# Kernel tuning notes

Measured on AMD Instinct MI355X. Metric: run time of the kernel, lower is better.

## Reference

```python
import jax, jax.numpy as jnp
import numpy as np

D_MODEL = 2048
NUM_HEADS = 16
D_KV = D_MODEL // NUM_HEADS
THETA = 10000.0


def apply_rope(x, pos):
    # x: [B, H, S, d_kv], pos: [S] int
    d = x.shape[-1]
    inv_freq = 1.0 / (THETA ** (jnp.arange(0, d, 2, dtype=jnp.float32) / d))  # [d/2]
    ang = pos.astype(jnp.float32)[:, None] * inv_freq[None, :]  # [S, d/2]
    cos, sin = jnp.cos(ang), jnp.sin(ang)  # broadcast over B,H
    x1 = x[..., 0::2]
    x2 = x[..., 1::2]
    r1 = x1 * cos - x2 * sin
    r2 = x1 * sin + x2 * cos
    return jnp.stack([r1, r2], axis=-1).reshape(x.shape)


def setup_inputs() -> dict:
    key = jax.random.key(0)
    k = jax.random.split(key, 5)
    B, S = 2, 2048
    x = jax.random.normal(k[0], (B, S, D_MODEL), dtype=jnp.float32)
    scale = 1.0 / np.sqrt(D_MODEL)
    Wq = jax.random.normal(k[1], (D_MODEL, D_MODEL), dtype=jnp.float32) * scale
    Wk = jax.random.normal(k[2], (D_MODEL, D_MODEL), dtype=jnp.float32) * scale
    Wv = jax.random.normal(k[3], (D_MODEL, D_MODEL), dtype=jnp.float32) * scale
    Wo = jax.random.normal(k[4], (D_MODEL, D_MODEL), dtype=jnp.float32) * scale
    token_position = jnp.arange(S, dtype=jnp.int64 if jax.config.jax_enable_x64 else jnp.int32)
    return {"x": x, "Wq": Wq, "Wk": Wk, "Wv": Wv, "Wo": Wo, "token_position": token_position}


def reference(x, Wq, Wk, Wv, Wo, token_position):
    B, S, _ = x.shape
    def heads(y):
        return y.reshape(B, S, NUM_HEADS, D_KV).transpose(0, 2, 1, 3)  # [B,H,S,d]
    Q = heads(jnp.einsum('bsd,df->bsf', x, Wq))
    K = heads(jnp.einsum('bsd,df->bsf', x, Wk))
    V = heads(jnp.einsum('bsd,df->bsf', x, Wv))
    Q = apply_rope(Q, token_position)
    K = apply_rope(K, token_position)
    scale = 1.0 / jnp.sqrt(jnp.asarray(D_KV, dtype=x.dtype))
    scores = jnp.einsum('bhqd,bhkd->bhqk', Q, K) * scale  # [B,H,S,S]
    causal = jnp.tril(jnp.ones((S, S), dtype=bool))
    scores = jnp.where(causal, scores, -jnp.inf)
    attn = jax.nn.softmax(scores, axis=-1)
    out = jnp.einsum('bhqk,bhkd->bhqd', attn, V)  # [B,H,S,d]
    out = out.transpose(0, 2, 1, 3).reshape(B, S, D_MODEL)
    return jnp.einsum('bsd,df->bsf', out, Wo)
```

## Files before the change

### kernel.cpp

```cpp
#include <hip/hip_runtime.h>
#include <hip/hip_bf16.h>

#define S 2048
#define DM 2048
#define NH 16
#define DH 128

typedef __attribute__((ext_vector_type(8))) short short8;
typedef __attribute__((ext_vector_type(4))) float floatx4;
typedef unsigned short u16;
typedef unsigned int u32;

__device__ __forceinline__ u16 f2bf(float f) {
  union { float f; u32 u; } v; v.f = f;
  u32 r = v.u + 0x7fffu + ((v.u >> 16) & 1u);
  return (u16)(r >> 16);
}
__device__ __forceinline__ u32 pack2(float lo, float hi) {
  float2 f; f.x = lo; f.y = hi;
  __hip_bfloat162 h = __float22bfloat162_rn(f);
  union { __hip_bfloat162 h; u32 u; } c; c.h = h;
  return c.u;
}

__device__ __forceinline__ floatx4 mfma16(short8 a, short8 b, floatx4 c) {
  return __builtin_amdgcn_mfma_f32_16x16x32_bf16(a, b, c, 0, 0, 0);
}

__device__ __forceinline__ void async_cp16(const u16* g, u16* l) {
  __builtin_amdgcn_global_load_lds(
      (const __attribute__((address_space(1))) void*)g,
      (__attribute__((address_space(3))) void*)l, 16, 0, 0);
}

__global__ void conv_x_k(const float* __restrict__ x, u16* __restrict__ xb) {
  int gid = blockIdx.x * 256 + threadIdx.x;
  float4 v = ((const float4*)x)[gid];
  uint2 p; p.x = pack2(v.x, v.y); p.y = pack2(v.z, v.w);
  ((uint2*)xb)[gid] = p;
}

__global__ void conv_w_k(const float* __restrict__ W0, const float* __restrict__ W1,
                         const float* __restrict__ W2, const float* __restrict__ W3,
                         u16* __restrict__ out) {
  __shared__ float tile[32][33];
  const float* W = blockIdx.z == 0 ? W0 : blockIdx.z == 1 ? W1 : blockIdx.z == 2 ? W2 : W3;
  u16* O = out + (size_t)blockIdx.z * DM * DM;
  int tx = threadIdx.x & 31, ty = threadIdx.x >> 5;
  int k0 = blockIdx.y * 32, n0 = blockIdx.x * 32;
#pragma unroll
  for (int j = 0; j < 4; j++)
    tile[ty + j * 8][tx] = W[(size_t)(k0 + ty + j * 8) * DM + n0 + tx];
  __syncthreads();
#pragma unroll
  for (int j = 0; j < 4; j++)
    O[(size_t)(n0 + ty + j * 8) * DM + k0 + tx] = f2bf(tile[tx][ty + j * 8]);
}

#define BM 256
#define BN 128
#define BK 64
#define NT (DM / BK)

#define STAGE(p, koff) do {                       \
    async_cp16(pA0 + (koff), &As[p][oA0]);        \
    async_cp16(pA1 + (koff), &As[p][oA1]);        \
    async_cp16(pA2 + (koff), &As[p][oA2]);        \
    async_cp16(pA3 + (koff), &As[p][oA3]);        \
    async_cp16(pB0 + (koff), &Bs[p][oB0]);        \
    async_cp16(pB1 + (koff), &Bs[p][oB1]);        \
  } while (0)

#define PHASE(p, g, F) {                                                  \
    short8 a0k0 = *(const short8*)&As[p][arow64 + (2*(g))*1024 + xk0];    \
    short8 a0k1 = *(const short8*)&As[p][arow64 + (2*(g))*1024 + xk1];    \
    short8 a1k0 = *(const short8*)&As[p][arow64 + (2*(g)+1)*1024 + xk0];  \
    short8 a1k1 = *(const short8*)&As[p][arow64 + (2*(g)+1)*1024 + xk1];  \
    if (F) {                                                              \
      bA = *(const short8*)&Bs[p][brow64 + xk0];                          \
      bB = *(const short8*)&Bs[p][brow64 + xk1];                          \
      bC = *(const short8*)&Bs[p][brow64 + 1024 + xk0];                   \
      bD = *(const short8*)&Bs[p][brow64 + 1024 + xk1];                   \
    }                                                                     \
    __builtin_amdgcn_s_barrier();                                         \
    asm volatile("s_waitcnt lgkmcnt(0)" ::: "memory");                    \
    __builtin_amdgcn_sched_barrier(0);                                    \
    __builtin_amdgcn_s_setprio(1);                                        \
    acc[2*(g)][0]   = mfma16(a0k0, bA, acc[2*(g)][0]);                    \
    acc[2*(g)][1]   = mfma16(a0k0, bC, acc[2*(g)][1]);                    \
    acc[2*(g)+1][0] = mfma16(a1k0, bA, acc[2*(g)+1][0]);                  \
    acc[2*(g)+1][1] = mfma16(a1k0, bC, acc[2*(g)+1][1]);                  \
    acc[2*(g)][0]   = mfma16(a0k1, bB, acc[2*(g)][0]);                    \
    acc[2*(g)][1]   = mfma16(a0k1, bD, acc[2*(g)][1]);                    \
    acc[2*(g)+1][0] = mfma16(a1k1, bB, acc[2*(g)+1][0]);                  \
    acc[2*(g)+1][1] = mfma16(a1k1, bD, acc[2*(g)+1][1]);                  \
    __builtin_amdgcn_s_setprio(0);                                        \
    __builtin_amdgcn_s_barrier();                                         \
  }

#define BOUNDARY(p, koff, pre) {                                          \
    __builtin_amdgcn_sched_barrier(0);                                    \
    if (pre) {                                                            \
      STAGE(p, koff);                                                     \
      __builtin_amdgcn_sched_barrier(0);                                  \
      asm volatile("s_waitcnt vmcnt(6)" ::: "memory");                    \
    } else {                                                              \
      asm volatile("s_waitcnt vmcnt(0)" ::: "memory");                    \
    }                                                                     \
    __builtin_amdgcn_s_barrier();                                         \
    __builtin_amdgcn_sched_barrier(0);                                    \
  }

__global__ __launch_bounds__(512, 2)
void gemm_k(const u16* __restrict__ A, const u16* __restrict__ Wt,
            u16* __restrict__ oQ, u16* __restrict__ oK, u16* __restrict__ oV,
            float* __restrict__ oO, const int* __restrict__ tp, int opmode)
{
  __shared__ u16 As[2][BM * BK];
  __shared__ u16 Bs[2][BN * BK];
  const int t = threadIdx.x;
  const int w = t >> 6, lane = t & 63;
  const int l16 = lane & 15, quad = lane >> 4;
  const int wr = w >> 2, wc = w & 3;
  const int m0 = blockIdx.y * BM, n0 = blockIdx.x * BN;
  const u16* Bt = Wt + (size_t)(opmode == 1 ? 3 : blockIdx.z) * DM * DM;

  int uu, rr, cc;
  uu = t;        rr = uu >> 3; cc = (uu & 7) ^ (rr & 7);
  const u16* pA0 = A + (size_t)(m0 + rr) * DM + cc * 8; const int oA0 = uu * 8;
  uu = t + 512;  rr = uu >> 3; cc = (uu & 7) ^ (rr & 7);
  const u16* pA1 = A + (size_t)(m0 + rr) * DM + cc * 8; const int oA1 = uu * 8;
  uu = t + 1024; rr = uu >> 3; cc = (uu & 7) ^ (rr & 7);
  const u16* pA2 = A + (size_t)(m0 + rr) * DM + cc * 8; const int oA2 = uu * 8;
  uu = t + 1536; rr = uu >> 3; cc = (uu & 7) ^ (rr & 7);
  const u16* pA3 = A + (size_t)(m0 + rr) * DM + cc * 8; const int oA3 = uu * 8;
  uu = t;        rr = uu >> 3; cc = (uu & 7) ^ (rr & 7);
  const u16* pB0 = Bt + (size_t)(n0 + rr) * DM + cc * 8; const int oB0 = uu * 8;
  uu = t + 512;  rr = uu >> 3; cc = (uu & 7) ^ (rr & 7);
  const u16* pB1 = Bt + (size_t)(n0 + rr) * DM + cc * 8; const int oB1 = uu * 8;

  const int arow64 = (wr * 128 + l16) * 64;
  const int brow64 = (wc * 32 + l16) * 64;
  const int xk0 = ((quad) ^ (l16 & 7)) << 3;
  const int xk1 = ((4 + quad) ^ (l16 & 7)) << 3;

  floatx4 acc[8][2] = {};
  short8 bA, bB, bC, bD;

  STAGE(0, 0);
  STAGE(1, BK);
  __builtin_amdgcn_sched_barrier(0);
  asm volatile("s_waitcnt vmcnt(6)" ::: "memory");
  __builtin_amdgcn_s_barrier();
  __builtin_amdgcn_sched_barrier(0);

  for (int it = 0; it < NT / 2; ++it) {
    const int koffE = it * 128 + 128;
    const int koffO = it * 128 + 192;
    const bool pre = (it < NT / 2 - 1);
    PHASE(0, 0, 1) PHASE(0, 1, 0) PHASE(0, 2, 0) PHASE(0, 3, 0)
    BOUNDARY(0, koffE, pre)
    PHASE(1, 0, 1) PHASE(1, 1, 0) PHASE(1, 2, 0) PHASE(1, 3, 0)
    BOUNDARY(1, koffO, pre)
  }

  const int mode = (opmode == 1) ? 3 : ((int)blockIdx.z == 2 ? 2 : 0);
  const int mbase = m0 + wr * 128;
  const int nbase = n0 + wc * 32;
  if (mode == 3) {
#pragma unroll
    for (int mi = 0; mi < 8; mi++) {
      int m = mbase + mi * 16 + quad * 4;
#pragma unroll
      for (int ni = 0; ni < 2; ni++) {
        int n = nbase + ni * 16 + l16;
#pragma unroll
        for (int r = 0; r < 4; r++)
          oO[(size_t)(m + r) * DM + n] = acc[mi][ni][r];
      }
    }
  } else if (mode == 2) {
#pragma unroll
    for (int mi = 0; mi < 8; mi++) {
      int m = mbase + mi * 16 + quad * 4;
      int b = m >> 11, s = m & (S - 1);
#pragma unroll
      for (int ni = 0; ni < 2; ni++) {
        int f = nbase + ni * 16 + l16;
        int h = f >> 7, dh = f & (DH - 1);
        uint2 pk; pk.x = pack2(acc[mi][ni][0], acc[mi][ni][1]);
        pk.y = pack2(acc[mi][ni][2], acc[mi][ni][3]);
        *(uint2*)&oV[((size_t)(b * NH + h) * DH + dh) * S + s] = pk;
      }
    }
  } else {
    u16* Out = ((int)blockIdx.z == 0) ? oQ : oK;
    const float qs = ((int)blockIdx.z == 0) ? 0.12752780f : 1.0f;
#pragma unroll
    for (int mi = 0; mi < 8; mi++) {
#pragma unroll
      for (int r = 0; r < 4; r++) {
        int m = mbase + mi * 16 + quad * 4 + r;
        int b = m >> 11, s = m & (S - 1);
        int ps = tp[s];
#pragma unroll
        for (int ni = 0; ni < 2; ni++) {
          int f = nbase + ni * 16 + l16;
          int h = f >> 7, dh = f & (DH - 1);
          float own = acc[mi][ni][r];
          float oth = __shfl_xor(own, 1, 64);
          float fr = __expf((float)(dh & ~1) * (-9.210340371976184f / 128.0f));
          float ang = (float)ps * fr;
          float sn, cs; __sincosf(ang, &sn, &cs);
          float res = (dh & 1) ? (oth * sn + own * cs) : (own * cs - oth * sn);
          Out[((size_t)(b * NH + h) * S + s) * DH + dh] = f2bf(res * qs);
        }
      }
    }
  }
}

__global__ __launch_bounds__(256, 4)
void attn_k(const u16* __restrict__ Q, const u16* __restrict__ K,
            const u16* __restrict__ Vt, u16* __restrict__ O)
{
  __shared__ u16 Ks[64 * 128];
  __shared__ u16 Vs[128 * 64];
  __shared__ u16 P[4][16 * 64];
  const int t = threadIdx.x, w = t >> 6, lane = t & 63;
  const int l16 = lane & 15, quad = lane >> 4;
  const int task = blockIdx.x;
  const int bh = task & 31, b = bh >> 4, h = bh & 15;
  const int g = 31 - (task >> 5);
  const int qg = g * 64;
  const int qt = qg + w * 16;
  const u16* Qb = Q + (size_t)bh * S * DH;
  const u16* Kb = K + (size_t)bh * S * DH;
  const u16* Vb = Vt + (size_t)bh * DH * S;
  u16* Pw = P[w];
  const int pxor = l16 & 7;

  const u16* pK[4]; u16* lK[4];
  const u16* pV[4]; u16* lV[4];
#pragma unroll
  for (int j = 0; j < 4; j++) {
    int kr = w * 16 + j * 4 + (lane >> 4);
    int ks = lane & 15;
    int kc = ks ^ (kr & 15);
    pK[j] = Kb + (size_t)kr * DH + kc * 8;
    lK[j] = &Ks[kr * 128 + ks * 8];
    int vr = w * 32 + j * 8 + (lane >> 3);
    int vs = lane & 7;
    int vc = vs ^ (vr & 7);
    pV[j] = Vb + (size_t)vr * S + vc * 8;
    lV[j] = &Vs[vr * 64 + vs * 8];
  }

  short8 aq[4];
#pragma unroll
  for (int kc = 0; kc < 4; kc++)
    aq[kc] = *(const short8*)&Qb[(size_t)(qt + l16) * DH + kc * 32 + quad * 8];

  floatx4 o[8] = {};
  float lsum = 0.0f;
  const int kend = qg + 64;

  for (int k0 = 0; k0 < kend; k0 += 64) {
#pragma unroll
    for (int j = 0; j < 4; j++) async_cp16(pK[j] + (size_t)k0 * DH, lK[j]);
#pragma unroll
    for (int j = 0; j < 4; j++) async_cp16(pV[j] + k0, lV[j]);
    __syncthreads();

    floatx4 sc[4] = {};
#pragma unroll
    for (int hh = 0; hh < 4; hh++) {
      int row = hh * 16 + l16;
#pragma unroll
      for (int kc = 0; kc < 4; kc++) {
        short8 kf = *(short8*)&Ks[row * 128 + (((kc * 4 + quad) ^ l16) << 3)];
        sc[hh] = mfma16(kf, aq[kc], sc[hh]);
      }
    }
    if (k0 + 64 > qt) {
#pragma unroll
      for (int hh = 0; hh < 4; hh++)
#pragma unroll
        for (int r = 0; r < 4; r++) {
          int j = k0 + hh * 16 + quad * 4 + r;
          if (j > qt + l16) sc[hh][r] = -3.0e38f;
        }
    }
#pragma unroll
    for (int hh = 0; hh < 4; hh++) {
      float e0 = __builtin_amdgcn_exp2f(fminf(sc[hh][0], 44.0f));
      float e1 = __builtin_amdgcn_exp2f(fminf(sc[hh][1], 44.0f));
      float e2 = __builtin_amdgcn_exp2f(fminf(sc[hh][2], 44.0f));
      float e3 = __builtin_amdgcn_exp2f(fminf(sc[hh][3], 44.0f));
      lsum += (e0 + e1) + (e2 + e3);
      uint2 pk; pk.x = pack2(e0, e1); pk.y = pack2(e2, e3);
      int su = (2 * hh + (quad >> 1)) ^ pxor;
      *(uint2*)&Pw[l16 * 64 + su * 8 + (quad & 1) * 4] = pk;
    }
    asm volatile("s_waitcnt lgkmcnt(0)" ::: "memory");
#pragma unroll
    for (int c = 0; c < 2; c++) {
      short8 pf = *(short8*)&Pw[l16 * 64 + (((4 * c + quad) ^ pxor) << 3)];
#pragma unroll
      for (int t8 = 0; t8 < 8; t8++) {
        int row = t8 * 16 + l16;
        short8 av = *(short8*)&Vs[row * 64 + (((c * 4 + quad) ^ (l16 & 7)) << 3)];
        o[t8] = mfma16(av, pf, o[t8]);
      }
    }
    __syncthreads();
  }

  float l = lsum + __shfl_xor(lsum, 16, 64);
  l += __shfl_xor(l, 32, 64);
  float inv = __builtin_amdgcn_rcpf(l);
#pragma unroll
  for (int t8 = 0; t8 < 8; t8++) {
    uint2 pa;
    pa.x = pack2(o[t8][0] * inv, o[t8][1] * inv);
    pa.y = pack2(o[t8][2] * inv, o[t8][3] * inv);
    *(uint2*)&O[((size_t)(b * S + qt + l16)) * DM + h * DH + t8 * 16 + quad * 4] = pa;
  }
}

extern "C" void kernel_launch(void* const* d_in, const int* in_sizes, int n_in,
                              void* d_out, int out_size, void* d_ws, size_t ws_size,
                              hipStream_t stream) {
  const float* x  = (const float*)d_in[0];
  const float* Wq = (const float*)d_in[1];
  const float* Wk = (const float*)d_in[2];
  const float* Wv = (const float*)d_in[3];
  const float* Wo = (const float*)d_in[4];
  const int*   tp = (const int*)d_in[5];

  char* ws = (char*)d_ws;
  u16* Wt = (u16*)ws;
  u16* xb = (u16*)(ws + 33554432);
  u16* Qb = (u16*)(ws + 50331648);
  u16* Kb = (u16*)(ws + 67108864);
  u16* Vb = (u16*)(ws + 83886080);
  u16* Ob = (u16*)(ws + 100663296);

  conv_x_k<<<8192, 256, 0, stream>>>(x, xb);
  conv_w_k<<<dim3(64, 64, 4), 256, 0, stream>>>(Wq, Wk, Wv, Wo, Wt);
  gemm_k<<<dim3(DM / BN, 4096 / BM, 3), 512, 0, stream>>>(xb, Wt, Qb, Kb, Vb,
                                                          nullptr, tp, 0);
  attn_k<<<1024, 256, 0, stream>>>(Qb, Kb, Vb, Ob);
  gemm_k<<<dim3(DM / BN, 4096 / BM, 1), 512, 0, stream>>>(Ob, Wt, nullptr, nullptr,
                                                          nullptr, (float*)d_out, tp, 1);
}
```

Before: 383.3 us.

## Reshape GEMM warp tiling from 128x32 to 64x64 per wave

Changes the wave layout in the projection GEMM from a 2x4 grid with 128x32 tiles per wave to a 4x2 grid with 64x64 tiles. Each k-step, a wave now loads four A fragments and eight B fragments instead of eight A and four B, and the work is split into two phases of 16 MFMAs each instead of four phases of 8. The squarer tile is meant to cut LDS read traffic per MFMA and halve the barrier count per k-tile. In exchange, more B fragments stay live in registers, which adds register pressure under the 2-blocks-per-CU launch bound.

```diff
diff --git a/kernel.cpp b/kernel.cpp
--- a/kernel.cpp
+++ b/kernel.cpp
@@ -71,29 +71,68 @@
     async_cp16(pB1 + (koff), &Bs[p][oB1]);        \
   } while (0)
 
-#define PHASE(p, g, F) {                                                  \
-    short8 a0k0 = *(const short8*)&As[p][arow64 + (2*(g))*1024 + xk0];    \
-    short8 a0k1 = *(const short8*)&As[p][arow64 + (2*(g))*1024 + xk1];    \
-    short8 a1k0 = *(const short8*)&As[p][arow64 + (2*(g)+1)*1024 + xk0];  \
-    short8 a1k1 = *(const short8*)&As[p][arow64 + (2*(g)+1)*1024 + xk1];  \
-    if (F) {                                                              \
-      bA = *(const short8*)&Bs[p][brow64 + xk0];                          \
-      bB = *(const short8*)&Bs[p][brow64 + xk1];                          \
-      bC = *(const short8*)&Bs[p][brow64 + 1024 + xk0];                   \
-      bD = *(const short8*)&Bs[p][brow64 + 1024 + xk1];                   \
-    }                                                                     \
+#define PHASE0(p) {                                                       \
+    short8 a0k0 = *(const short8*)&As[p][abase + xk0];                    \
+    short8 a0k1 = *(const short8*)&As[p][abase + xk1];                    \
+    short8 a1k0 = *(const short8*)&As[p][abase + 1024 + xk0];             \
+    short8 a1k1 = *(const short8*)&As[p][abase + 1024 + xk1];             \
+    b00 = *(const short8*)&Bs[p][bbase + xk0];                            \
+    b01 = *(const short8*)&Bs[p][bbase + xk1];                            \
+    b10 = *(const short8*)&Bs[p][bbase + 1024 + xk0];                     \
+    b11 = *(const short8*)&Bs[p][bbase + 1024 + xk1];                     \
+    b20 = *(const short8*)&Bs[p][bbase + 2048 + xk0];                     \
+    b21 = *(const short8*)&Bs[p][bbase + 2048 + xk1];                     \
+    b30 = *(const short8*)&Bs[p][bbase + 3072 + xk0];                     \
+    b31 = *(const short8*)&Bs[p][bbase + 3072 + xk1];                     \
     __builtin_amdgcn_s_barrier();                                         \
     asm volatile("s_waitcnt lgkmcnt(0)" ::: "memory");                    \
     __builtin_amdgcn_sched_barrier(0);                                    \
     __builtin_amdgcn_s_setprio(1);                                        \
-    acc[2*(g)][0]   = mfma16(a0k0, bA, acc[2*(g)][0]);                    \
-    acc[2*(g)][1]   = mfma16(a0k0, bC, acc[2*(g)][1]);                    \
-    acc[2*(g)+1][0] = mfma16(a1k0, bA, acc[2*(g)+1][0]);                  \
-    acc[2*(g)+1][1] = mfma16(a1k0, bC, acc[2*(g)+1][1]);                  \
-    acc[2*(g)][0]   = mfma16(a0k1, bB, acc[2*(g)][0]);                    \
-    acc[2*(g)][1]   = mfma16(a0k1, bD, acc[2*(g)][1]);                    \
-    acc[2*(g)+1][0] = mfma16(a1k1, bB, acc[2*(g)+1][0]);                  \
-    acc[2*(g)+1][1] = mfma16(a1k1, bD, acc[2*(g)+1][1]);                  \
+    acc[0][0] = mfma16(a0k0, b00, acc[0][0]);                             \
+    acc[0][1] = mfma16(a0k0, b10, acc[0][1]);                             \
+    acc[0][2] = mfma16(a0k0, b20, acc[0][2]);                             \
+    acc[0][3] = mfma16(a0k0, b30, acc[0][3]);                             \
+    acc[1][0] = mfma16(a1k0, b00, acc[1][0]);                             \
+    acc[1][1] = mfma16(a1k0, b10, acc[1][1]);                             \
+    acc[1][2] = mfma16(a1k0, b20, acc[1][2]);                             \
+    acc[1][3] = mfma16(a1k0, b30, acc[1][3]);                             \
+    acc[0][0] = mfma16(a0k1, b01, acc[0][0]);                             \
+    acc[0][1] = mfma16(a0k1, b11, acc[0][1]);                             \
+    acc[0][2] = mfma16(a0k1, b21, acc[0][2]);                             \
+    acc[0][3] = mfma16(a0k1, b31, acc[0][3]);                             \
+    acc[1][0] = mfma16(a1k1, b01, acc[1][0]);                             \
+    acc[1][1] = mfma16(a1k1, b11, acc[1][1]);                             \
+    acc[1][2] = mfma16(a1k1, b21, acc[1][2]);                             \
+    acc[1][3] = mfma16(a1k1, b31, acc[1][3]);                             \
+    __builtin_amdgcn_s_setprio(0);                                        \
+    __builtin_amdgcn_s_barrier();                                         \
+  }
+
+#define PHASE1(p) {                                                       \
+    short8 a2k0 = *(const short8*)&As[p][abase + 2048 + xk0];             \
+    short8 a2k1 = *(const short8*)&As[p][abase + 2048 + xk1];             \
+    short8 a3k0 = *(const short8*)&As[p][abase + 3072 + xk0];             \
+    short8 a3k1 = *(const short8*)&As[p][abase + 3072 + xk1];             \
+    __builtin_amdgcn_s_barrier();                                         \
+    asm volatile("s_waitcnt lgkmcnt(0)" ::: "memory");                    \
+    __builtin_amdgcn_sched_barrier(0);                                    \
+    __builtin_amdgcn_s_setprio(1);                                        \
+    acc[2][0] = mfma16(a2k0, b00, acc[2][0]);                             \
+    acc[2][1] = mfma16(a2k0, b10, acc[2][1]);                             \
+    acc[2][2] = mfma16(a2k0, b20, acc[2][2]);                             \
+    acc[2][3] = mfma16(a2k0, b30, acc[2][3]);                             \
+    acc[3][0] = mfma16(a3k0, b00, acc[3][0]);                             \
+    acc[3][1] = mfma16(a3k0, b10, acc[3][1]);                             \
+    acc[3][2] = mfma16(a3k0, b20, acc[3][2]);                             \
+    acc[3][3] = mfma16(a3k0, b30, acc[3][3]);                             \
+    acc[2][0] = mfma16(a2k1, b01, acc[2][0]);                             \
+    acc[2][1] = mfma16(a2k1, b11, acc[2][1]);                             \
+    acc[2][2] = mfma16(a2k1, b21, acc[2][2]);                             \
+    acc[2][3] = mfma16(a2k1, b31, acc[2][3]);                             \
+    acc[3][0] = mfma16(a3k1, b01, acc[3][0]);                             \
+    acc[3][1] = mfma16(a3k1, b11, acc[3][1]);                             \
+    acc[3][2] = mfma16(a3k1, b21, acc[3][2]);                             \
+    acc[3][3] = mfma16(a3k1, b31, acc[3][3]);                             \
     __builtin_amdgcn_s_setprio(0);                                        \
     __builtin_amdgcn_s_barrier();                                         \
   }
@@ -121,7 +160,7 @@
   const int t = threadIdx.x;
   const int w = t >> 6, lane = t & 63;
   const int l16 = lane & 15, quad = lane >> 4;
-  const int wr = w >> 2, wc = w & 3;
+  const int wr = w >> 1, wc = w & 1;
   const int m0 = blockIdx.y * BM, n0 = blockIdx.x * BN;
   const u16* Bt = Wt + (size_t)(opmode == 1 ? 3 : blockIdx.z) * DM * DM;
 
@@ -139,13 +178,13 @@
   uu = t + 512;  rr = uu >> 3; cc = (uu & 7) ^ (rr & 7);
   const u16* pB1 = Bt + (size_t)(n0 + rr) * DM + cc * 8; const int oB1 = uu * 8;
 
-  const int arow64 = (wr * 128 + l16) * 64;
-  const int brow64 = (wc * 32 + l16) * 64;
+  const int abase = (wr * 64 + l16) * 64;
+  const int bbase = (wc * 64 + l16) * 64;
   const int xk0 = ((quad) ^ (l16 & 7)) << 3;
   const int xk1 = ((4 + quad) ^ (l16 & 7)) << 3;
 
-  floatx4 acc[8][2] = {};
-  short8 bA, bB, bC, bD;
+  floatx4 acc[4][4] = {};
+  short8 b00, b01, b10, b11, b20, b21, b30, b31;
 
   STAGE(0, 0);
   STAGE(1, BK);
@@ -158,21 +197,21 @@
     const int koffE = it * 128 + 128;
     const int koffO = it * 128 + 192;
     const bool pre = (it < NT / 2 - 1);
-    PHASE(0, 0, 1) PHASE(0, 1, 0) PHASE(0, 2, 0) PHASE(0, 3, 0)
+    PHASE0(0) PHASE1(0)
     BOUNDARY(0, koffE, pre)
-    PHASE(1, 0, 1) PHASE(1, 1, 0) PHASE(1, 2, 0) PHASE(1, 3, 0)
+    PHASE0(1) PHASE1(1)
     BOUNDARY(1, koffO, pre)
   }
 
   const int mode = (opmode == 1) ? 3 : ((int)blockIdx.z == 2 ? 2 : 0);
-  const int mbase = m0 + wr * 128;
-  const int nbase = n0 + wc * 32;
+  const int mbase = m0 + wr * 64;
+  const int nbase = n0 + wc * 64;
   if (mode == 3) {
 #pragma unroll
-    for (int mi = 0; mi < 8; mi++) {
+    for (int mi = 0; mi < 4; mi++) {
       int m = mbase + mi * 16 + quad * 4;
 #pragma unroll
-      for (int ni = 0; ni < 2; ni++) {
+      for (int ni = 0; ni < 4; ni++) {
         int n = nbase + ni * 16 + l16;
 #pragma unroll
         for (int r = 0; r < 4; r++)
@@ -181,11 +220,11 @@
     }
   } else if (mode == 2) {
 #pragma unroll
-    for (int mi = 0; mi < 8; mi++) {
+    for (int mi = 0; mi < 4; mi++) {
       int m = mbase + mi * 16 + quad * 4;
       int b = m >> 11, s = m & (S - 1);
 #pragma unroll
-      for (int ni = 0; ni < 2; ni++) {
+      for (int ni = 0; ni < 4; ni++) {
         int f = nbase + ni * 16 + l16;
         int h = f >> 7, dh = f & (DH - 1);
         uint2 pk; pk.x = pack2(acc[mi][ni][0], acc[mi][ni][1]);
@@ -197,14 +236,14 @@
     u16* Out = ((int)blockIdx.z == 0) ? oQ : oK;
     const float qs = ((int)blockIdx.z == 0) ? 0.12752780f : 1.0f;
 #pragma unroll
-    for (int mi = 0; mi < 8; mi++) {
+    for (int mi = 0; mi < 4; mi++) {
 #pragma unroll
       for (int r = 0; r < 4; r++) {
         int m = mbase + mi * 16 + quad * 4 + r;
         int b = m >> 11, s = m & (S - 1);
         int ps = tp[s];
 #pragma unroll
-        for (int ni = 0; ni < 2; ni++) {
+        for (int ni = 0; ni < 4; ni++) {
           int f = nbase + ni * 16 + l16;
           int h = f >> 7, dh = f & (DH - 1);
           float own = acc[mi][ni][r];
```

After: 380.5 us. Within noise of the previous version (-0.7%).
